# Optimization experiments

Measured on AMD Instinct MI355X. Metric: run time of the kernel, lower is better.

Reference implementation:

```python
import jax, jax.numpy as jnp
import numpy as np

D_MODEL, H, D_FF = 1024, 16, 4096
D_K = D_MODEL // H
EPS = 1e-6
NEG = -1e9


def _layer_norm(x, alpha, bias):
    # torch LayerNormalization: scalar alpha/bias, unbiased std (ddof=1), eps added to std
    n = x.shape[-1]
    mu = jnp.mean(x, axis=-1, keepdims=True)
    var = jnp.sum((x - mu) ** 2, axis=-1, keepdims=True) / (n - 1)
    std = jnp.sqrt(var)
    return alpha * (x - mu) / (std + EPS) + bias


def _linear(x, w, b):
    # torch nn.Linear: y = x @ W^T + b, W: [out, in]
    return jnp.einsum('bsd,od->bso', x, w) + b


def setup_inputs() -> dict:
    key = jax.random.key(0)
    ks = jax.random.split(key, 12)
    d, dff = D_MODEL, D_FF
    s_d = 1.0 / np.sqrt(d)
    s_ff = 1.0 / np.sqrt(dff)
    inp = {
        'x': jax.random.normal(ks[0], (2, 2048, d), dtype=jnp.float32),
        'mask': jnp.ones((2, 1, 1, 2048), dtype=jnp.int32),
        'wq': jax.random.uniform(ks[1], (d, d), jnp.float32, -s_d, s_d),
        'bq': jnp.zeros((d,), jnp.float32),
        'wk': jax.random.uniform(ks[2], (d, d), jnp.float32, -s_d, s_d),
        'bk': jnp.zeros((d,), jnp.float32),
        'wv': jax.random.uniform(ks[3], (d, d), jnp.float32, -s_d, s_d),
        'bv': jnp.zeros((d,), jnp.float32),
        'wo': jax.random.uniform(ks[4], (d, d), jnp.float32, -s_d, s_d),
        'bo': jnp.zeros((d,), jnp.float32),
        'w1': jax.random.uniform(ks[5], (dff, d), jnp.float32, -s_d, s_d),
        'b1': jnp.zeros((dff,), jnp.float32),
        'w2': jax.random.uniform(ks[6], (d, dff), jnp.float32, -s_ff, s_ff),
        'b2': jnp.zeros((d,), jnp.float32),
        'ln1_a': jnp.ones((1,), jnp.float32),
        'ln1_b': jnp.zeros((1,), jnp.float32),
        'ln2_a': jnp.ones((1,), jnp.float32),
        'ln2_b': jnp.zeros((1,), jnp.float32),
    }
    return inp


def reference(x, mask, wq, bq, wk, bk, wv, bv, wo, bo, w1, b1, w2, b2,
              ln1_a, ln1_b, ln2_a, ln2_b):
    b, s, d = x.shape

    # --- residual 1: pre-norm self-attention (dropout is identity in eval) ---
    xn = _layer_norm(x, ln1_a, ln1_b)
    q = _linear(xn, wq, bq).reshape(b, s, H, D_K).transpose(0, 2, 1, 3)  # [b,h,s,dk]
    k = _linear(xn, wk, bk).reshape(b, s, H, D_K).transpose(0, 2, 1, 3)
    v = _linear(xn, wv, bv).reshape(b, s, H, D_K).transpose(0, 2, 1, 3)
    scores = jnp.einsum('bhqd,bhkd->bhqk', q, k) / jnp.sqrt(jnp.float32(D_K))
    scores = jnp.where(mask == 0, NEG, scores)
    p = jax.nn.softmax(scores, axis=-1)
    attn = jnp.einsum('bhqk,bhkd->bhqd', p, v)
    attn = attn.transpose(0, 2, 1, 3).reshape(b, s, d)
    x = x + _linear(attn, wo, bo)

    # --- residual 2: pre-norm feed-forward ---
    xn = _layer_norm(x, ln2_a, ln2_b)
    h = jax.nn.relu(_linear(xn, w1, b1))
    x = x + _linear(h, w2, b2)
    return x
```

## Files before the change

### kernel.cpp

```cpp
#include <hip/hip_runtime.h>
#include <hip/hip_bf16.h>
#include <stdint.h>

typedef __bf16 bf16x8 __attribute__((ext_vector_type(8)));
typedef __bf16 bf16x4 __attribute__((ext_vector_type(4)));
typedef short  s16x4  __attribute__((ext_vector_type(4)));
typedef float  f32x4  __attribute__((ext_vector_type(4)));
typedef unsigned short u16;

__device__ __forceinline__ u16 f2bf(float f) {
    return __builtin_bit_cast(u16, (__bf16)f);
}

__device__ __forceinline__ f32x4 vmax4(f32x4 a, f32x4 b) {
    f32x4 r;
    r[0] = fmaxf(a[0], b[0]); r[1] = fmaxf(a[1], b[1]);
    r[2] = fmaxf(a[2], b[2]); r[3] = fmaxf(a[3], b[3]);
    return r;
}
__device__ __forceinline__ f32x4 vexp4(f32x4 a) {
    f32x4 r;
    r[0] = __expf(a[0]); r[1] = __expf(a[1]);
    r[2] = __expf(a[2]); r[3] = __expf(a[3]);
    return r;
}

__device__ __forceinline__ f32x4 mfma16(bf16x4 a, bf16x4 b, f32x4 c) {
#if __has_builtin(__builtin_amdgcn_mfma_f32_16x16x16bf16_1k)
    return __builtin_amdgcn_mfma_f32_16x16x16bf16_1k(
        __builtin_bit_cast(s16x4, a), __builtin_bit_cast(s16x4, b), c, 0, 0, 0);
#else
    f32x4 d;
    asm volatile("v_mfma_f32_16x16x16_bf16 %0, %1, %2, %3"
                 : "=v"(d) : "v"(a), "v"(b), "v"(c));
    return d;
#endif
}

__device__ __forceinline__ void stage16(const void* g, void* lds_wave_base) {
#if __has_builtin(__builtin_amdgcn_global_load_lds)
    __builtin_amdgcn_global_load_lds(
        (const __attribute__((address_space(1))) void*)g,
        (__attribute__((address_space(3))) void*)lds_wave_base, 16, 0, 0);
#else
    int lane = threadIdx.x & 63;
    *(uint4*)((char*)lds_wave_base + lane * 16) = *(const uint4*)g;
#endif
}

__device__ __forceinline__ int swz(int r) {
    return (((r) & 7) ^ (((r) >> 3) & 7)) << 4;
}

__global__ void pack1_kernel(const float* __restrict__ wq, const float* __restrict__ wk,
                             const float* __restrict__ wv, const float* __restrict__ bq,
                             const float* __restrict__ bk, const float* __restrict__ bv,
                             const float* __restrict__ wo,
                             u16* __restrict__ wqkv, float* __restrict__ bqkv,
                             u16* __restrict__ wo_b) {
    const float QS = 0.125f;
    size_t i0 = (size_t)blockIdx.x * 256 + threadIdx.x;
    size_t stride = (size_t)gridDim.x * 256;
    const size_t DD = 1024u * 1024u;
    for (size_t i = i0; i < 3 * DD; i += stride) {
        float v;
        if (i < DD)          v = wq[i] * QS;
        else if (i < 2 * DD) v = wk[i - DD];
        else                 v = wv[i - 2 * DD];
        wqkv[i] = f2bf(v);
    }
    for (size_t i = i0; i < DD; i += stride) wo_b[i] = f2bf(wo[i]);
    for (size_t i = i0; i < 3072; i += stride)
        bqkv[i] = (i < 1024) ? bq[i] * QS : ((i < 2048) ? bk[i - 1024] : bv[i - 2048]);
}

__global__ void pack2_kernel(const float* __restrict__ w1, const float* __restrict__ w2,
                             u16* __restrict__ w1_b, u16* __restrict__ w2_b) {
    size_t i0 = (size_t)blockIdx.x * 256 + threadIdx.x;
    size_t stride = (size_t)gridDim.x * 256;
    const size_t DD = 1024u * 1024u;
    for (size_t i = i0; i < 4 * DD; i += stride) w1_b[i] = f2bf(w1[i]);
    for (size_t i = i0; i < 4 * DD; i += stride) w2_b[i] = f2bf(w2[i]);
}

__global__ __launch_bounds__(256)
void ln_kernel(const float* __restrict__ x, u16* __restrict__ out,
               const float* __restrict__ alpha, const float* __restrict__ beta) {
    const int row = blockIdx.x;
    const int t = threadIdx.x, lane = t & 63, w = t >> 6;
    float4 v = ((const float4*)(x + (size_t)row * 1024))[t];
    float s  = v.x + v.y + v.z + v.w;
    float ss = v.x * v.x + v.y * v.y + v.z * v.z + v.w * v.w;
#pragma unroll
    for (int d = 1; d < 64; d <<= 1) { s += __shfl_xor(s, d); ss += __shfl_xor(ss, d); }
    __shared__ float red[8];
    if (lane == 0) { red[w] = s; red[4 + w] = ss; }
    __syncthreads();
    s  = red[0] + red[1] + red[2] + red[3];
    ss = red[4] + red[5] + red[6] + red[7];
    const float mu  = s * (1.f / 1024.f);
    const float var = fmaxf((ss - 1024.f * mu * mu) * (1.f / 1023.f), 0.f);
    const float inv = alpha[0] / (sqrtf(var) + 1e-6f);
    const float bb  = beta[0];
    ushort4 o;
    o.x = f2bf((v.x - mu) * inv + bb);
    o.y = f2bf((v.y - mu) * inv + bb);
    o.z = f2bf((v.z - mu) * inv + bb);
    o.w = f2bf((v.w - mu) * inv + bb);
    ((ushort4*)(out + (size_t)row * 1024))[t] = o;
}

template <int EPI>
__global__ __launch_bounds__(256)
void gemm_bt(const u16* __restrict__ A, const u16* __restrict__ B,
             const float* __restrict__ bias, const float* __restrict__ resid,
             void* __restrict__ Cout, int M, int N, int K, int ldc) {
    __shared__ __align__(16) char As[16384];
    __shared__ __align__(16) char Bs[16384];
    const int t = threadIdx.x;
    const int lane = t & 63, wave = t >> 6;
    const int g = lane >> 4, c = lane & 15;
    const int wm = wave >> 1, wn = wave & 1;
    const int bm = blockIdx.x, bn = blockIdx.y;

    const f32x4 z4 = {0.f, 0.f, 0.f, 0.f};
    f32x4 acc[4][4];
#pragma unroll
    for (int m = 0; m < 4; ++m)
#pragma unroll
        for (int n = 0; n < 4; ++n) acc[m][n] = z4;

    const int srow = t >> 2;
    const int ak = (((t & 3) ^ ((t >> 2) & 3)) << 3);
    const u16* ga = A + (size_t)(bm * 128 + srow) * K + ak;
    const u16* gb = B + (size_t)(bn * 128 + srow) * K + ak;
    const size_t rstep = (size_t)64 * K;

    auto STAGE = [&](int k0, int buf) {
        char* la = As + buf * 8192 + wave * 1024;
        char* lb = Bs + buf * 8192 + wave * 1024;
        stage16(ga + k0,         la);
        stage16(ga + k0 + rstep, la + 4096);
        stage16(gb + k0,         lb);
        stage16(gb + k0 + rstep, lb + 4096);
    };

    STAGE(0, 0);
    asm volatile("s_waitcnt vmcnt(0)" ::: "memory");
    __syncthreads();

    int cur = 0;
    for (int k0 = 0; k0 < K; k0 += 32) {
        if (k0 + 32 < K) STAGE(k0 + 32, cur ^ 1);
        const char* Ac = As + cur * 8192;
        const char* Bc = Bs + cur * 8192;
        bf16x8 a[4], b[4];
#pragma unroll
        for (int m = 0; m < 4; ++m) {
            int r = wm * 64 + m * 16 + c;
            a[m] = *(const bf16x8*)(Ac + r * 64 + ((g * 16) ^ ((c & 3) << 4)));
        }
#pragma unroll
        for (int n = 0; n < 4; ++n) {
            int r = wn * 64 + n * 16 + c;
            b[n] = *(const bf16x8*)(Bc + r * 64 + ((g * 16) ^ ((c & 3) << 4)));
        }
        __builtin_amdgcn_s_setprio(1);
#pragma unroll
        for (int m = 0; m < 4; ++m)
#pragma unroll
            for (int n = 0; n < 4; ++n)
                acc[m][n] = __builtin_amdgcn_mfma_f32_16x16x32_bf16(a[m], b[n], acc[m][n], 0, 0, 0);
        __builtin_amdgcn_s_setprio(0);
        asm volatile("s_waitcnt vmcnt(0)" ::: "memory");
        __syncthreads();
        cur ^= 1;
    }

    const int row0 = bm * 128 + wm * 64;
    const int col0 = bn * 128 + wn * 64;
#pragma unroll
    for (int m = 0; m < 4; ++m) {
#pragma unroll
        for (int n = 0; n < 4; ++n) {
            const int cc = col0 + n * 16 + c;
            const float bv = bias[cc];
#pragma unroll
            for (int j = 0; j < 4; ++j) {
                const int rr = row0 + m * 16 + g * 4 + j;
                float v = acc[m][n][j] + bv;
                if (EPI == 1) v = v > 0.f ? v : 0.f;
                if (EPI == 2) {
                    ((float*)Cout)[(size_t)rr * ldc + cc] = resid[(size_t)rr * ldc + cc] + v;
                } else {
                    ((u16*)Cout)[(size_t)rr * ldc + cc] = f2bf(v);
                }
            }
        }
    }
}

template <int EPI>
__global__ __launch_bounds__(512)
void gemm256(const u16* __restrict__ A, const u16* __restrict__ B,
             const float* __restrict__ bias, u16* __restrict__ Cout,
             int K, int ldc, int gm) {
    extern __shared__ __align__(16) char lds[];
    char* As0 = lds;
    char* Bs0 = lds + 65536;
    const int t = threadIdx.x, lane = t & 63, wave = t >> 6;
    const int g = lane >> 4, c = lane & 15;
    const int wm = wave >> 2, wn = wave & 3;
    const int f = blockIdx.x, nb = gridDim.x;
    const int sw = (f & 7) * (nb >> 3) + (f >> 3);
    const int bm = sw % gm, bn = sw / gm;

    const f32x4 z4 = {0.f, 0.f, 0.f, 0.f};
    f32x4 acc[8][4];
#pragma unroll
    for (int mi = 0; mi < 8; ++mi)
#pragma unroll
        for (int ni = 0; ni < 4; ++ni) acc[mi][ni] = z4;

    auto STAGE = [&](const u16* G, int base_row, int k0, char* dst, int half) {
#pragma unroll
        for (int l = 0; l < 2; ++l) {
            int idx = half * 1024 + l * 512 + t;
            int row = idx >> 3, p = idx & 7;
            stage16(G + (size_t)(base_row + row) * K + k0 + ((p ^ (row & 7)) << 3),
                    dst + (half * 1024 + l * 512 + wave * 64) * 16);
        }
    };
    auto ldA = [&](int buf, int mi, int ks) -> bf16x8 {
        int r = wm * 128 + mi * 16 + c;
        return *(const bf16x8*)(As0 + buf * 32768 + r * 128 + ((((ks << 2) + g) ^ (r & 7)) << 4));
    };
    auto ldB = [&](int buf, int ni, int ks) -> bf16x8 {
        int r = wn * 64 + ni * 16 + c;
        return *(const bf16x8*)(Bs0 + buf * 32768 + r * 128 + ((((ks << 2) + g) ^ (r & 7)) << 4));
    };

    const int NT = K >> 6;
    STAGE(A, bm * 256, 0, As0, 0); STAGE(A, bm * 256, 0, As0, 1);
    STAGE(B, bn * 256, 0, Bs0, 0); STAGE(B, bn * 256, 0, Bs0, 1);
    asm volatile("s_waitcnt vmcnt(0)" ::: "memory");
    __builtin_amdgcn_s_barrier();

    int cur = 0;
    for (int kt = 0; kt < NT; ++kt) {
        const int k0n = (kt + 1) << 6;
        const bool more = kt + 1 < NT;
        bf16x8 bfr[4][2];
#pragma unroll
        for (int ni = 0; ni < 4; ++ni) {
            bfr[ni][0] = ldB(cur, ni, 0);
            bfr[ni][1] = ldB(cur, ni, 1);
        }
#pragma unroll
        for (int ph = 0; ph < 4; ++ph) {
            bf16x8 a0k0 = ldA(cur, 2 * ph, 0),     a0k1 = ldA(cur, 2 * ph, 1);
            bf16x8 a1k0 = ldA(cur, 2 * ph + 1, 0), a1k1 = ldA(cur, 2 * ph + 1, 1);
            if (more && ph == 0) {
                STAGE(A, bm * 256, k0n, As0 + (cur ^ 1) * 32768, 0);
                STAGE(A, bm * 256, k0n, As0 + (cur ^ 1) * 32768, 1);
            }
            if (more && ph == 1) {
                STAGE(B, bn * 256, k0n, Bs0 + (cur ^ 1) * 32768, 0);
                STAGE(B, bn * 256, k0n, Bs0 + (cur ^ 1) * 32768, 1);
            }
            __builtin_amdgcn_s_barrier();
            __builtin_amdgcn_s_setprio(1);
#pragma unroll
            for (int ni = 0; ni < 4; ++ni) {
                acc[2 * ph][ni]     = __builtin_amdgcn_mfma_f32_16x16x32_bf16(a0k0, bfr[ni][0], acc[2 * ph][ni], 0, 0, 0);
                acc[2 * ph][ni]     = __builtin_amdgcn_mfma_f32_16x16x32_bf16(a0k1, bfr[ni][1], acc[2 * ph][ni], 0, 0, 0);
                acc[2 * ph + 1][ni] = __builtin_amdgcn_mfma_f32_16x16x32_bf16(a1k0, bfr[ni][0], acc[2 * ph + 1][ni], 0, 0, 0);
                acc[2 * ph + 1][ni] = __builtin_amdgcn_mfma_f32_16x16x32_bf16(a1k1, bfr[ni][1], acc[2 * ph + 1][ni], 0, 0, 0);
            }
            __builtin_amdgcn_s_setprio(0);
            __builtin_amdgcn_s_barrier();
        }
        asm volatile("s_waitcnt vmcnt(0)" ::: "memory");
        __builtin_amdgcn_s_barrier();
        cur ^= 1;
    }

    const int row0 = bm * 256 + wm * 128;
    const int col0 = bn * 256 + wn * 64;
#pragma unroll
    for (int mi = 0; mi < 8; ++mi) {
#pragma unroll
        for (int ni = 0; ni < 4; ++ni) {
            const int cc = col0 + ni * 16 + c;
            const float bv = bias[cc];
#pragma unroll
            for (int j = 0; j < 4; ++j) {
                const int rr = row0 + mi * 16 + g * 4 + j;
                float v = acc[mi][ni][j] + bv;
                if (EPI == 1) v = v > 0.f ? v : 0.f;
                Cout[(size_t)rr * ldc + cc] = f2bf(v);
            }
        }
    }
}

__global__ __launch_bounds__(256)
void attn_kernel(const u16* __restrict__ qkv, const int* __restrict__ mask,
                 u16* __restrict__ attn_out) {
    __shared__ __align__(16) char Ksm[32768];
    __shared__ __align__(16) char Vsm[16384];
    const int t = threadIdx.x, lane = t & 63, w = t >> 6;
    const int g = lane >> 4, c = lane & 15;
    const int flat = blockIdx.x;
    const int xcd = flat & 7, u = flat >> 3;
    const int qt = u & 31;
    const int p = xcd * 4 + (u >> 5);
    const int h = p & 15, b = p >> 4;
    const int S = 2048, LD = 3072;
    const int NT = S / 128;

    bf16x8 qf[2];
#pragma unroll
    for (int half = 0; half < 2; ++half)
        qf[half] = *(const bf16x8*)&qkv[(size_t)(b * S + qt * 64 + w * 16 + c) * LD
                                        + h * 64 + half * 32 + g * 8];

    const f32x4 z4 = {0.f, 0.f, 0.f, 0.f};
    f32x4 accO[4];
#pragma unroll
    for (int dt = 0; dt < 4; ++dt) accO[dt] = z4;
    float mrun = -1e30f, lrun = 0.f;

    unsigned vr[2][8];
    const int vd0 = (t & 31) * 2;
    const int vkg[2] = {t >> 5, 8 + (t >> 5)};

    auto STAGEK = [&](int kt, char* Kd) {
#pragma unroll
        for (int it = 0; it < 4; ++it) {
            int idx = it * 256 + t;
            int k = idx >> 3, pp = idx & 7;
            int ps = pp ^ ((k & 7) ^ ((k >> 3) & 7));
            stage16(&qkv[(size_t)(b * S + kt * 128 + k) * LD + 1024 + h * 64 + ps * 8],
                    Kd + (it * 256 + w * 64) * 16);
        }
    };
    auto VLOAD = [&](int kt) {
#pragma unroll
        for (int it = 0; it < 2; ++it) {
            const u16* src = &qkv[(size_t)(b * S + kt * 128 + vkg[it] * 8) * LD + 2048 + h * 64 + vd0];
#pragma unroll
            for (int i = 0; i < 8; ++i)
                vr[it][i] = *(const unsigned*)(src + (size_t)i * LD);
        }
    };
    auto VWRITE = [&]() {
#pragma unroll
        for (int it = 0; it < 2; ++it) {
            int d0 = vd0, kg = vkg[it];
            uint4 lo, hi;
            lo.x = (vr[it][0] & 0xffffu) | (vr[it][1] << 16);
            lo.y = (vr[it][2] & 0xffffu) | (vr[it][3] << 16);
            lo.z = (vr[it][4] & 0xffffu) | (vr[it][5] << 16);
            lo.w = (vr[it][6] & 0xffffu) | (vr[it][7] << 16);
            hi.x = (vr[it][0] >> 16) | (vr[it][1] & 0xffff0000u);
            hi.y = (vr[it][2] >> 16) | (vr[it][3] & 0xffff0000u);
            hi.z = (vr[it][4] >> 16) | (vr[it][5] & 0xffff0000u);
            hi.w = (vr[it][6] >> 16) | (vr[it][7] & 0xffff0000u);
            *(uint4*)(Vsm + d0 * 256 + ((kg * 16) ^ swz(d0)))           = lo;
            *(uint4*)(Vsm + (d0 + 1) * 256 + ((kg * 16) ^ swz(d0 + 1))) = hi;
        }
    };

    STAGEK(0, Ksm);
    VLOAD(0);
    asm volatile("s_waitcnt vmcnt(0)" ::: "memory");
    VWRITE();
    __syncthreads();

    int cur = 0;
    for (int kt = 0; kt < NT; ++kt) {
        char* Kc = Ksm + cur * 16384;
        if (kt + 1 < NT) {
            STAGEK(kt + 1, Ksm + (cur ^ 1) * 16384);
            VLOAD(kt + 1);
        }

        f32x4 s[8];
        __builtin_amdgcn_s_setprio(1);
#pragma unroll
        for (int n = 0; n < 8; ++n) {
            int kr = n * 16 + c;
            bf16x8 k0 = *(const bf16x8*)(Kc + kr * 128 + ((g * 16) ^ swz(kr)));
            bf16x8 k1 = *(const bf16x8*)(Kc + kr * 128 + ((64 + g * 16) ^ swz(kr)));
            s[n] = __builtin_amdgcn_mfma_f32_16x16x32_bf16(k0, qf[0], z4, 0, 0, 0);
            s[n] = __builtin_amdgcn_mfma_f32_16x16x32_bf16(k1, qf[1], s[n], 0, 0, 0);
        }
        __builtin_amdgcn_s_setprio(0);
#pragma unroll
        for (int n = 0; n < 8; ++n) {
            int4 mv = *(const int4*)&mask[b * S + kt * 128 + n * 16 + g * 4];
            if (mv.x == 0) s[n][0] = -1e9f;
            if (mv.y == 0) s[n][1] = -1e9f;
            if (mv.z == 0) s[n][2] = -1e9f;
            if (mv.w == 0) s[n][3] = -1e9f;
        }
        {
            f32x4 pm4 = s[0];
#pragma unroll
            for (int n = 1; n < 8; ++n) pm4 = vmax4(pm4, s[n]);
            float pm = fmaxf(fmaxf(pm4[0], pm4[1]), fmaxf(pm4[2], pm4[3]));
            pm = fmaxf(pm, __shfl_xor(pm, 16));
            pm = fmaxf(pm, __shfl_xor(pm, 32));
            float mn = fmaxf(mrun, pm);
            float sc = __expf(mrun - mn);
            mrun = mn;
            f32x4 mn4 = {mn, mn, mn, mn};
            f32x4 ps4 = z4;
#pragma unroll
            for (int n = 0; n < 8; ++n) { s[n] = vexp4(s[n] - mn4); ps4 += s[n]; }
            float ps = ps4[0] + ps4[1] + ps4[2] + ps4[3];
            ps += __shfl_xor(ps, 16);
            ps += __shfl_xor(ps, 32);
            lrun = lrun * sc + ps;
#pragma unroll
            for (int dt = 0; dt < 4; ++dt) accO[dt] *= sc;
        }
        __builtin_amdgcn_s_setprio(1);
#pragma unroll
        for (int n = 0; n < 8; ++n) {
            bf16x4 p0;
#pragma unroll
            for (int j = 0; j < 4; ++j) p0[j] = (__bf16)s[n][j];
#pragma unroll
            for (int dt = 0; dt < 4; ++dt) {
                int d = dt * 16 + c;
                bf16x4 vf = *(const bf16x4*)(Vsm + d * 256 + ((n * 32 + g * 8) ^ swz(d)));
                accO[dt] = mfma16(vf, p0, accO[dt]);
            }
        }
        __builtin_amdgcn_s_setprio(0);

        __syncthreads();
        asm volatile("s_waitcnt vmcnt(0)" ::: "memory");
        if (kt + 1 < NT) VWRITE();
        __syncthreads();
        cur ^= 1;
    }

    char* Osm = Ksm;
    {
        float inv = 1.f / lrun;
        int ql = w * 16 + c;
#pragma unroll
        for (int dt = 0; dt < 4; ++dt)
#pragma unroll
            for (int j = 0; j < 4; ++j) {
                int d = dt * 16 + g * 4 + j;
                *(u16*)(Osm + ql * 128 + ((d * 2) ^ swz(ql))) = f2bf(accO[dt][j] * inv);
            }
    }
    __syncthreads();
#pragma unroll
    for (int it = 0; it < 2; ++it) {
        int idx = it * 256 + t;
        int q = idx >> 3, pp = idx & 7;
        uint4 val = *(const uint4*)(Osm + q * 128 + ((pp * 16) ^ swz(q)));
        *(uint4*)&attn_out[(size_t)(b * S + qt * 64 + q) * 1024 + h * 64 + pp * 8] = val;
    }
}

extern "C" void kernel_launch(void* const* d_in, const int* in_sizes, int n_in,
                              void* d_out, int out_size, void* d_ws, size_t ws_size,
                              hipStream_t stream) {
    const float* x    = (const float*)d_in[0];
    const int*   mask = (const int*)d_in[1];
    const float* wq   = (const float*)d_in[2];
    const float* bq   = (const float*)d_in[3];
    const float* wk   = (const float*)d_in[4];
    const float* bk   = (const float*)d_in[5];
    const float* wv   = (const float*)d_in[6];
    const float* bv   = (const float*)d_in[7];
    const float* wo   = (const float*)d_in[8];
    const float* bo   = (const float*)d_in[9];
    const float* w1   = (const float*)d_in[10];
    const float* b1   = (const float*)d_in[11];
    const float* w2   = (const float*)d_in[12];
    const float* b2   = (const float*)d_in[13];
    const float* ln1a = (const float*)d_in[14];
    const float* ln1b = (const float*)d_in[15];
    const float* ln2a = (const float*)d_in[16];
    const float* ln2b = (const float*)d_in[17];

    const size_t MB = 1048576;
    char* ws = (char*)d_ws;
    const bool big = ws_size >= 88 * MB;

    hipFuncSetAttribute(reinterpret_cast<const void*>(gemm256<0>),
                        hipFuncAttributeMaxDynamicSharedMemorySize, 131072);
    hipFuncSetAttribute(reinterpret_cast<const void*>(gemm256<1>),
                        hipFuncAttributeMaxDynamicSharedMemorySize, 131072);

    u16 *xn, *wqkv, *wo_b, *qkvb, *attnb, *w1_b, *w2_b, *hbuf;
    float *bqkv, *x1;
    int nchunk;
    if (big) {
        xn    = (u16*)(ws + 0 * MB);
        wqkv  = (u16*)(ws + 8 * MB);
        wo_b  = (u16*)(ws + 14 * MB);
        qkvb  = (u16*)(ws + 16 * MB);
        attnb = (u16*)(ws + 40 * MB);
        x1    = (float*)(ws + 48 * MB);
        w1_b  = (u16*)(ws + 64 * MB);
        w2_b  = (u16*)(ws + 72 * MB);
        hbuf  = (u16*)(ws + 16 * MB);
        bqkv  = (float*)(ws + 80 * MB);
        nchunk = 1;
    } else {
        xn    = (u16*)(ws + 0 * MB);
        wqkv  = (u16*)(ws + 8 * MB);
        wo_b  = (u16*)(ws + 14 * MB);
        qkvb  = (u16*)(ws + 16 * MB);
        attnb = (u16*)(ws + 40 * MB);
        x1    = (float*)(ws + 16 * MB);
        w1_b  = (u16*)(ws + 32 * MB);
        w2_b  = (u16*)(ws + 8 * MB);
        hbuf  = (u16*)(ws + 40 * MB);
        bqkv  = (float*)(ws + 40 * MB);
        nchunk = 4;
    }

    pack1_kernel<<<1024, 256, 0, stream>>>(wq, wk, wv, bq, bk, bv, wo, wqkv, bqkv, wo_b);
    ln_kernel<<<4096, 256, 0, stream>>>(x, xn, ln1a, ln1b);
    gemm256<0><<<192, 512, 131072, stream>>>(xn, wqkv, bqkv, qkvb, 1024, 3072, 16);
    attn_kernel<<<1024, 256, 0, stream>>>(qkvb, mask, attnb);
    gemm_bt<2><<<dim3(32, 8), 256, 0, stream>>>(attnb, wo_b, bo, x, x1,
                                                4096, 1024, 1024, 1024);
    pack2_kernel<<<1024, 256, 0, stream>>>(w1, w2, w1_b, w2_b);
    ln_kernel<<<4096, 256, 0, stream>>>(x1, xn, ln2a, ln2b);

    if (big) {
        gemm256<1><<<256, 512, 131072, stream>>>(xn, w1_b, b1, hbuf, 1024, 4096, 16);
        gemm_bt<2><<<dim3(32, 8), 256, 0, stream>>>(hbuf, w2_b, b2, x1, (float*)d_out,
                                                    4096, 1024, 4096, 1024);
    } else {
        const int mrows = 4096 / nchunk;
        for (int cidx = 0; cidx < nchunk; ++cidx) {
            const size_t ro = (size_t)cidx * mrows;
            gemm_bt<1><<<dim3(mrows / 128, 32), 256, 0, stream>>>(
                xn + ro * 1024, w1_b, b1, nullptr, hbuf, mrows, 4096, 1024, 4096);
            gemm_bt<2><<<dim3(mrows / 128, 8), 256, 0, stream>>>(
                hbuf, w2_b, b2, x1 + ro * 1024, (float*)d_out + ro * 1024,
                mrows, 1024, 4096, 1024);
        }
    }
}
```

Measured before the change: 298.1 us.

## Fuse weight packing, precompute mask flags, use exp2 softmax, add 8-wave GEMM

```diff
diff --git a/kernel.cpp b/kernel.cpp
--- a/kernel.cpp
+++ b/kernel.cpp
@@ -18,10 +18,10 @@
     r[2] = fmaxf(a[2], b[2]); r[3] = fmaxf(a[3], b[3]);
     return r;
 }
-__device__ __forceinline__ f32x4 vexp4(f32x4 a) {
+__device__ __forceinline__ f32x4 vexp2_4(f32x4 a) {
     f32x4 r;
-    r[0] = __expf(a[0]); r[1] = __expf(a[1]);
-    r[2] = __expf(a[2]); r[3] = __expf(a[3]);
+    r[0] = exp2f(a[0]); r[1] = exp2f(a[1]);
+    r[2] = exp2f(a[2]); r[3] = exp2f(a[3]);
     return r;
 }
 
@@ -52,13 +52,16 @@
     return (((r) & 7) ^ (((r) >> 3) & 7)) << 4;
 }
 
-__global__ void pack1_kernel(const float* __restrict__ wq, const float* __restrict__ wk,
-                             const float* __restrict__ wv, const float* __restrict__ bq,
-                             const float* __restrict__ bk, const float* __restrict__ bv,
-                             const float* __restrict__ wo,
-                             u16* __restrict__ wqkv, float* __restrict__ bqkv,
-                             u16* __restrict__ wo_b) {
-    const float QS = 0.125f;
+__global__ void pack_kernel(const float* __restrict__ wq, const float* __restrict__ wk,
+                            const float* __restrict__ wv, const float* __restrict__ bq,
+                            const float* __restrict__ bk, const float* __restrict__ bv,
+                            const float* __restrict__ wo, const float* __restrict__ w1,
+                            const float* __restrict__ w2, const int* __restrict__ mask,
+                            u16* __restrict__ wqkv, float* __restrict__ bqkv,
+                            u16* __restrict__ wo_b, u16* __restrict__ w1_b,
+                            u16* __restrict__ w2_b, unsigned* __restrict__ flags,
+                            int do_ffn) {
+    const float QS = 0.125f * 1.44269504088896f;
     size_t i0 = (size_t)blockIdx.x * 256 + threadIdx.x;
     size_t stride = (size_t)gridDim.x * 256;
     const size_t DD = 1024u * 1024u;
@@ -70,8 +73,25 @@
         wqkv[i] = f2bf(v);
     }
     for (size_t i = i0; i < DD; i += stride) wo_b[i] = f2bf(wo[i]);
+    if (do_ffn) {
+        for (size_t i = i0; i < 4 * DD; i += stride) w1_b[i] = f2bf(w1[i]);
+        for (size_t i = i0; i < 4 * DD; i += stride) w2_b[i] = f2bf(w2[i]);
+    }
     for (size_t i = i0; i < 3072; i += stride)
         bqkv[i] = (i < 1024) ? bq[i] * QS : ((i < 2048) ? bk[i - 1024] : bv[i - 2048]);
+    if (i0 < 2) {
+        unsigned fm = 0;
+        for (int kt = 0; kt < 16; ++kt) {
+            const int4* mp = (const int4*)(mask + i0 * 2048 + kt * 128);
+            int all1 = 1;
+            for (int j = 0; j < 32; ++j) {
+                int4 mv = mp[j];
+                all1 &= (mv.x != 0) & (mv.y != 0) & (mv.z != 0) & (mv.w != 0);
+            }
+            fm |= (unsigned)all1 << kt;
+        }
+        flags[i0] = fm;
+    }
 }
 
 __global__ void pack2_kernel(const float* __restrict__ w1, const float* __restrict__ w2,
@@ -202,6 +222,91 @@
 
 template <int EPI>
 __global__ __launch_bounds__(512)
+void gemm_bt8(const u16* __restrict__ A, const u16* __restrict__ B,
+              const float* __restrict__ bias, const float* __restrict__ resid,
+              void* __restrict__ Cout, int M, int N, int K, int ldc) {
+    __shared__ __align__(16) char As[16384];
+    __shared__ __align__(16) char Bs[16384];
+    const int t = threadIdx.x;
+    const int lane = t & 63, wave = t >> 6;
+    const int g = lane >> 4, c = lane & 15;
+    const int wm = wave >> 2, wn = wave & 3;
+    const int bm = blockIdx.x, bn = blockIdx.y;
+
+    const f32x4 z4 = {0.f, 0.f, 0.f, 0.f};
+    f32x4 acc[4][2];
+#pragma unroll
+    for (int m = 0; m < 4; ++m)
+#pragma unroll
+        for (int n = 0; n < 2; ++n) acc[m][n] = z4;
+
+    const int srow = t >> 2;
+    const int ak = (((t & 3) ^ ((t >> 2) & 3)) << 3);
+    const u16* ga = A + (size_t)(bm * 128 + srow) * K + ak;
+    const u16* gb = B + (size_t)(bn * 128 + srow) * K + ak;
+
+    auto STAGE = [&](int k0, int buf) {
+        stage16(ga + k0, As + buf * 8192 + wave * 1024);
+        stage16(gb + k0, Bs + buf * 8192 + wave * 1024);
+    };
+
+    STAGE(0, 0);
+    asm volatile("s_waitcnt vmcnt(0)" ::: "memory");
+    __syncthreads();
+
+    int cur = 0;
+    for (int k0 = 0; k0 < K; k0 += 32) {
+        if (k0 + 32 < K) STAGE(k0 + 32, cur ^ 1);
+        const char* Ac = As + cur * 8192;
+        const char* Bc = Bs + cur * 8192;
+        bf16x8 a[4], b[2];
+#pragma unroll
+        for (int m = 0; m < 4; ++m) {
+            int r = wm * 64 + m * 16 + c;
+            a[m] = *(const bf16x8*)(Ac + r * 64 + ((g * 16) ^ ((c & 3) << 4)));
+        }
+#pragma unroll
+        for (int n = 0; n < 2; ++n) {
+            int r = wn * 32 + n * 16 + c;
+            b[n] = *(const bf16x8*)(Bc + r * 64 + ((g * 16) ^ ((c & 3) << 4)));
+        }
+        __builtin_amdgcn_s_setprio(1);
+#pragma unroll
+        for (int m = 0; m < 4; ++m)
+#pragma unroll
+            for (int n = 0; n < 2; ++n)
+                acc[m][n] = __builtin_amdgcn_mfma_f32_16x16x32_bf16(a[m], b[n], acc[m][n], 0, 0, 0);
+        __builtin_amdgcn_s_setprio(0);
+        asm volatile("s_waitcnt vmcnt(0)" ::: "memory");
+        __syncthreads();
+        cur ^= 1;
+    }
+
+    const int row0 = bm * 128 + wm * 64;
+    const int col0 = bn * 128 + wn * 32;
+#pragma unroll
+    for (int m = 0; m < 4; ++m) {
+#pragma unroll
+        for (int n = 0; n < 2; ++n) {
+            const int cc = col0 + n * 16 + c;
+            const float bv = bias[cc];
+#pragma unroll
+            for (int j = 0; j < 4; ++j) {
+                const int rr = row0 + m * 16 + g * 4 + j;
+                float v = acc[m][n][j] + bv;
+                if (EPI == 1) v = v > 0.f ? v : 0.f;
+                if (EPI == 2) {
+                    ((float*)Cout)[(size_t)rr * ldc + cc] = resid[(size_t)rr * ldc + cc] + v;
+                } else {
+                    ((u16*)Cout)[(size_t)rr * ldc + cc] = f2bf(v);
+                }
+            }
+        }
+    }
+}
+
+template <int EPI>
+__global__ __launch_bounds__(512)
 void gemm256(const u16* __restrict__ A, const u16* __restrict__ B,
              const float* __restrict__ bias, u16* __restrict__ Cout,
              int K, int ldc, int gm) {
@@ -306,7 +411,7 @@
 
 __global__ __launch_bounds__(256)
 void attn_kernel(const u16* __restrict__ qkv, const int* __restrict__ mask,
-                 u16* __restrict__ attn_out) {
+                 const unsigned* __restrict__ flags, u16* __restrict__ attn_out) {
     __shared__ __align__(16) char Ksm[32768];
     __shared__ __align__(16) char Vsm[16384];
     const int t = threadIdx.x, lane = t & 63, w = t >> 6;
@@ -318,6 +423,8 @@
     const int h = p & 15, b = p >> 4;
     const int S = 2048, LD = 3072;
     const int NT = S / 128;
+
+    const unsigned fmask = flags[b];
 
     bf16x8 qf[2];
 #pragma unroll
@@ -397,13 +504,15 @@
             s[n] = __builtin_amdgcn_mfma_f32_16x16x32_bf16(k1, qf[1], s[n], 0, 0, 0);
         }
         __builtin_amdgcn_s_setprio(0);
-#pragma unroll
-        for (int n = 0; n < 8; ++n) {
-            int4 mv = *(const int4*)&mask[b * S + kt * 128 + n * 16 + g * 4];
-            if (mv.x == 0) s[n][0] = -1e9f;
-            if (mv.y == 0) s[n][1] = -1e9f;
-            if (mv.z == 0) s[n][2] = -1e9f;
-            if (mv.w == 0) s[n][3] = -1e9f;
+        if (!((fmask >> kt) & 1)) {
+#pragma unroll
+            for (int n = 0; n < 8; ++n) {
+                int4 mv = *(const int4*)&mask[b * S + kt * 128 + n * 16 + g * 4];
+                if (mv.x == 0) s[n][0] = -1e9f;
+                if (mv.y == 0) s[n][1] = -1e9f;
+                if (mv.z == 0) s[n][2] = -1e9f;
+                if (mv.w == 0) s[n][3] = -1e9f;
+            }
         }
         {
             f32x4 pm4 = s[0];
@@ -413,12 +522,12 @@
             pm = fmaxf(pm, __shfl_xor(pm, 16));
             pm = fmaxf(pm, __shfl_xor(pm, 32));
             float mn = fmaxf(mrun, pm);
-            float sc = __expf(mrun - mn);
+            float sc = exp2f(mrun - mn);
             mrun = mn;
             f32x4 mn4 = {mn, mn, mn, mn};
             f32x4 ps4 = z4;
 #pragma unroll
-            for (int n = 0; n < 8; ++n) { s[n] = vexp4(s[n] - mn4); ps4 += s[n]; }
+            for (int n = 0; n < 8; ++n) { s[n] = vexp2_4(s[n] - mn4); ps4 += s[n]; }
             float ps = ps4[0] + ps4[1] + ps4[2] + ps4[3];
             ps += __shfl_xor(ps, 16);
             ps += __shfl_xor(ps, 32);
@@ -503,7 +612,7 @@
 
     u16 *xn, *wqkv, *wo_b, *qkvb, *attnb, *w1_b, *w2_b, *hbuf;
     float *bqkv, *x1;
-    int nchunk;
+    unsigned* flags;
     if (big) {
         xn    = (u16*)(ws + 0 * MB);
         wqkv  = (u16*)(ws + 8 * MB);
@@ -515,7 +624,7 @@
         w2_b  = (u16*)(ws + 72 * MB);
         hbuf  = (u16*)(ws + 16 * MB);
         bqkv  = (float*)(ws + 80 * MB);
-        nchunk = 1;
+        flags = (unsigned*)(ws + 80 * MB + 65536);
     } else {
         xn    = (u16*)(ws + 0 * MB);
         wqkv  = (u16*)(ws + 8 * MB);
@@ -527,25 +636,27 @@
         w2_b  = (u16*)(ws + 8 * MB);
         hbuf  = (u16*)(ws + 40 * MB);
         bqkv  = (float*)(ws + 40 * MB);
-        nchunk = 4;
-    }
-
-    pack1_kernel<<<1024, 256, 0, stream>>>(wq, wk, wv, bq, bk, bv, wo, wqkv, bqkv, wo_b);
+        flags = (unsigned*)(ws + 32 * MB);
+    }
+
+    pack_kernel<<<2048, 256, 0, stream>>>(wq, wk, wv, bq, bk, bv, wo, w1, w2, mask,
+                                          wqkv, bqkv, wo_b, w1_b, w2_b, flags,
+                                          big ? 1 : 0);
     ln_kernel<<<4096, 256, 0, stream>>>(x, xn, ln1a, ln1b);
     gemm256<0><<<192, 512, 131072, stream>>>(xn, wqkv, bqkv, qkvb, 1024, 3072, 16);
-    attn_kernel<<<1024, 256, 0, stream>>>(qkvb, mask, attnb);
-    gemm_bt<2><<<dim3(32, 8), 256, 0, stream>>>(attnb, wo_b, bo, x, x1,
-                                                4096, 1024, 1024, 1024);
-    pack2_kernel<<<1024, 256, 0, stream>>>(w1, w2, w1_b, w2_b);
+    attn_kernel<<<1024, 256, 0, stream>>>(qkvb, mask, flags, attnb);
+    gemm_bt8<2><<<dim3(32, 8), 512, 0, stream>>>(attnb, wo_b, bo, x, x1,
+                                                 4096, 1024, 1024, 1024);
     ln_kernel<<<4096, 256, 0, stream>>>(x1, xn, ln2a, ln2b);
 
     if (big) {
         gemm256<1><<<256, 512, 131072, stream>>>(xn, w1_b, b1, hbuf, 1024, 4096, 16);
-        gemm_bt<2><<<dim3(32, 8), 256, 0, stream>>>(hbuf, w2_b, b2, x1, (float*)d_out,
-                                                    4096, 1024, 4096, 1024);
+        gemm_bt8<2><<<dim3(32, 8), 512, 0, stream>>>(hbuf, w2_b, b2, x1, (float*)d_out,
+                                                     4096, 1024, 4096, 1024);
     } else {
-        const int mrows = 4096 / nchunk;
-        for (int cidx = 0; cidx < nchunk; ++cidx) {
+        pack2_kernel<<<1024, 256, 0, stream>>>(w1, w2, w1_b, w2_b);
+        const int mrows = 1024;
+        for (int cidx = 0; cidx < 4; ++cidx) {
             const size_t ro = (size_t)cidx * mrows;
             gemm_bt<1><<<dim3(mrows / 128, 32), 256, 0, stream>>>(
                 xn + ro * 1024, w1_b, b1, nullptr, hbuf, mrows, 4096, 1024, 4096);
```

After: 316.7 us. +6.2%, slower.
